# Kernel tuning notes

Measured on AMD Instinct MI355X. Metric: run time of the kernel, lower is better.

## Reference

```python
import jax, jax.numpy as jnp
import numpy as np
import math

B, T, D, H = 16, 512, 1024, 16
DK = D // H
MAX_LEN = 512          # RelativePositionBias default
LOCAL_WINDOW = 128


def setup_inputs() -> dict:
    key = jax.random.key(0)
    ks = jax.random.split(key, 6)
    x = jax.random.normal(ks[0], (B, T, D), dtype=jnp.float32)
    Wqkv = jax.random.normal(ks[1], (D, 3 * D), dtype=jnp.float32) * 0.02
    bqkv = jnp.zeros((3 * D,), dtype=jnp.float32)
    Wo = jax.random.normal(ks[2], (D, D), dtype=jnp.float32) * 0.02
    bo = jnp.zeros((D,), dtype=jnp.float32)
    rel_table = jax.random.normal(ks[3], (2 * MAX_LEN - 1, H), dtype=jnp.float32) * 0.02
    return {"x": x, "Wqkv": Wqkv, "bqkv": bqkv, "Wo": Wo, "bo": bo, "rel_table": rel_table}


def reference(x, Wqkv, bqkv, Wo, bo, rel_table):
    # QKV projection: [B,T,3D]
    qkv = x @ Wqkv + bqkv
    q, k, v = jnp.split(qkv, 3, axis=-1)
    # [B,T,D] -> [B,H,T,DK]
    def to_heads(t):
        return t.reshape(B, T, H, DK).transpose(0, 2, 1, 3)
    q, k, v = to_heads(q), to_heads(k), to_heads(v)

    # scaled dot-product scores: [B,H,T,T]
    scores = jnp.einsum('bhqd,bhkd->bhqk', q, k) / math.sqrt(DK)

    # relative position bias: dist[i,j] = j - i, clipped index in [0, 2*max_len-2]
    r = jnp.arange(T)
    idx = (r[None, :] - r[:, None]) + (MAX_LEN - 1)   # [T,T]
    bias = rel_table[idx]                              # [T,T,H]
    scores = scores + bias.transpose(2, 0, 1)[None]    # [1,H,T,T]

    # local window mask: keep j in [i-w, i+w]
    keep = jnp.abs(r[:, None] - r[None, :]) <= LOCAL_WINDOW  # [T,T]
    scores = jnp.where(keep[None, None], scores, -jnp.inf)

    attn = jax.nn.softmax(scores, axis=-1)
    ctx = jnp.einsum('bhqk,bhkd->bhqd', attn, v)       # [B,H,T,DK]
    ctx = ctx.transpose(0, 2, 1, 3).reshape(B, T, D)
    out = ctx @ Wo + bo
    return (out, attn)
```

## Files before the change

### kernel.cpp

```cpp
#include <hip/hip_runtime.h>
#include <math.h>

typedef unsigned short ushort_t;
typedef __bf16 bf16x8 __attribute__((ext_vector_type(8)));
typedef float f32x4 __attribute__((ext_vector_type(4)));
typedef ushort_t u16x8 __attribute__((ext_vector_type(8)));

#define BB 16
#define TT 512
#define DD 1024
#define HH 16
#define DKK 64
#define WIN 128
#define MAXLEN 512

#define TILE_M 64
#define JSPAN 320
#define NCHUNK 5

#define BK 32
#define TBUF (128 * BK)
#define BUFU (4 * TBUF)
#define KSTEPS (DD / BK)

#define ALS 72

#define GLOAD16(g, l)                                                                              \
    __builtin_amdgcn_global_load_lds((const __attribute__((address_space(1))) unsigned int*)(g),   \
                                     (__attribute__((address_space(3))) unsigned int*)(l), 16, 0, 0)

__device__ __forceinline__ ushort_t f2bf(float f) {
    union { float f; unsigned u; } x; x.f = f;
    unsigned r = x.u + 0x7fffu + ((x.u >> 16) & 1u);
    return (ushort_t)(r >> 16);
}
__device__ __forceinline__ float bf2f(ushort_t h) {
    union { unsigned u; float f; } x; x.u = ((unsigned)h) << 16;
    return x.f;
}

__device__ __forceinline__ int swi(int row, int col) {
    return row * ALS + (col ^ (((row >> 3) & 7) << 3));
}

__global__ __launch_bounds__(256) void conv_split(const float* __restrict__ src,
                                                  ushort_t* __restrict__ hi,
                                                  ushort_t* __restrict__ lo, int n4)
{
    const int i = blockIdx.x * 256 + threadIdx.x;
    if (i >= n4) return;
    float4 vf = ((const float4*)src)[i];
    ushort_t h0 = f2bf(vf.x), h1 = f2bf(vf.y), h2 = f2bf(vf.z), h3 = f2bf(vf.w);
    ushort4 hv = make_ushort4(h0, h1, h2, h3);
    ushort4 lv = make_ushort4(f2bf(vf.x - bf2f(h0)), f2bf(vf.y - bf2f(h1)),
                              f2bf(vf.z - bf2f(h2)), f2bf(vf.w - bf2f(h3)));
    ((ushort4*)hi)[i] = hv;
    ((ushort4*)lo)[i] = lv;
}

__global__ __launch_bounds__(256) void conv_split_T(const float* __restrict__ W,
                                                    ushort_t* __restrict__ hiT,
                                                    ushort_t* __restrict__ loT,
                                                    int K, int N)
{
    __shared__ ushort_t th[32][33], tl[32][33];
    const int n0 = blockIdx.x * 32, k0 = blockIdx.y * 32;
    const int tid = threadIdx.x;
    const int r = tid >> 3, c4 = (tid & 7) * 4;
    float4 vf = *(const float4*)&W[(size_t)(k0 + r) * N + n0 + c4];
    float vv[4] = {vf.x, vf.y, vf.z, vf.w};
#pragma unroll
    for (int j = 0; j < 4; ++j) {
        ushort_t h = f2bf(vv[j]);
        th[r][c4 + j] = h;
        tl[r][c4 + j] = f2bf(vv[j] - bf2f(h));
    }
    __syncthreads();
    ushort4 oh = make_ushort4(th[c4 + 0][r], th[c4 + 1][r], th[c4 + 2][r], th[c4 + 3][r]);
    ushort4 ol = make_ushort4(tl[c4 + 0][r], tl[c4 + 1][r], tl[c4 + 2][r], tl[c4 + 3][r]);
    *(ushort4*)&hiT[(size_t)(n0 + r) * K + k0 + c4] = oh;
    *(ushort4*)&loT[(size_t)(n0 + r) * K + k0 + c4] = ol;
}

__device__ __forceinline__ void mfma_mainloop(const ushort_t* __restrict__ Ah,
                                              const ushort_t* __restrict__ Al,
                                              const ushort_t* __restrict__ Bh,
                                              const ushort_t* __restrict__ Bl,
                                              int m0, int n0,
                                              ushort_t* smem, f32x4 (&acc)[4][4])
{
    const int tid = threadIdx.x;
    const int lane = tid & 63;
    const int w = tid >> 6;
    const int wm = (w >> 1) * 64, wn = (w & 1) * 64;
    const int c16 = lane & 15;
    const int quad = lane >> 4;

    const int lrow = lane >> 2, lq = lane & 3;
    const int r0 = w * 32, r1 = w * 32 + 16;
    const int row0 = r0 + lrow, row1 = r1 + lrow;
    const int qd0 = lq ^ ((row0 >> 1) & 3);
    const int qd1 = lq ^ ((row1 >> 1) & 3);
    const size_t a0 = (size_t)(m0 + row0) * DD + qd0 * 8;
    const size_t a1 = (size_t)(m0 + row1) * DD + qd1 * 8;
    const size_t b0 = (size_t)(n0 + row0) * DD + qd0 * 8;
    const size_t b1 = (size_t)(n0 + row1) * DD + qd1 * 8;

    auto STAGE = [&](int buf, int k0) {
        ushort_t* s_ = smem + buf * BUFU;
        GLOAD16(Ah + a0 + k0, (char*)s_ + r0 * 64);
        GLOAD16(Ah + a1 + k0, (char*)s_ + r1 * 64);
        GLOAD16(Al + a0 + k0, (char*)(s_ + TBUF) + r0 * 64);
        GLOAD16(Al + a1 + k0, (char*)(s_ + TBUF) + r1 * 64);
        GLOAD16(Bh + b0 + k0, (char*)(s_ + 2 * TBUF) + r0 * 64);
        GLOAD16(Bh + b1 + k0, (char*)(s_ + 2 * TBUF) + r1 * 64);
        GLOAD16(Bl + b0 + k0, (char*)(s_ + 3 * TBUF) + r0 * 64);
        GLOAD16(Bl + b1 + k0, (char*)(s_ + 3 * TBUF) + r1 * 64);
    };

    int aoff[4], boff[4];
#pragma unroll
    for (int mt = 0; mt < 4; ++mt) {
        const int row = wm + mt * 16 + c16;
        aoff[mt] = row * BK + ((quad ^ ((row >> 1) & 3)) * 8);
    }
#pragma unroll
    for (int nt = 0; nt < 4; ++nt) {
        const int row = wn + nt * 16 + c16;
        boff[nt] = row * BK + ((quad ^ ((row >> 1) & 3)) * 8);
    }

    STAGE(0, 0);
    for (int t = 0; t < KSTEPS; ++t) {
        const int cur = t & 1;
        if (t + 1 < KSTEPS) {
            STAGE(cur ^ 1, (t + 1) * BK);
            asm volatile("s_waitcnt vmcnt(8)" ::: "memory");
        } else {
            asm volatile("s_waitcnt vmcnt(0)" ::: "memory");
        }
        __builtin_amdgcn_sched_barrier(0);
        __builtin_amdgcn_s_barrier();

        const ushort_t* sAh = smem + cur * BUFU;
        const ushort_t* sAl = sAh + TBUF;
        const ushort_t* sBh = sAh + 2 * TBUF;
        const ushort_t* sBl = sAh + 3 * TBUF;
        bf16x8 ah[4], al[4];
#pragma unroll
        for (int mt = 0; mt < 4; ++mt) {
            ah[mt] = *(const bf16x8*)&sAh[aoff[mt]];
            al[mt] = *(const bf16x8*)&sAl[aoff[mt]];
        }
#pragma unroll
        for (int nt = 0; nt < 4; ++nt) {
            bf16x8 bh = *(const bf16x8*)&sBh[boff[nt]];
            bf16x8 bl = *(const bf16x8*)&sBl[boff[nt]];
#pragma unroll
            for (int mt = 0; mt < 4; ++mt) {
                acc[mt][nt] = __builtin_amdgcn_mfma_f32_16x16x32_bf16(ah[mt], bh, acc[mt][nt], 0, 0, 0);
                acc[mt][nt] = __builtin_amdgcn_mfma_f32_16x16x32_bf16(al[mt], bh, acc[mt][nt], 0, 0, 0);
                acc[mt][nt] = __builtin_amdgcn_mfma_f32_16x16x32_bf16(ah[mt], bl, acc[mt][nt], 0, 0, 0);
            }
        }
        __builtin_amdgcn_sched_barrier(0);
        __builtin_amdgcn_s_barrier();
    }
}

__global__ __launch_bounds__(256) void qkv_mfma(const ushort_t* __restrict__ xh,
                                                const ushort_t* __restrict__ xl,
                                                const ushort_t* __restrict__ wh,
                                                const ushort_t* __restrict__ wl,
                                                const float* __restrict__ bias,
                                                ushort_t* __restrict__ qh,
                                                ushort_t* __restrict__ ql,
                                                ushort_t* __restrict__ kh,
                                                ushort_t* __restrict__ kl,
                                                ushort_t* __restrict__ vh,
                                                ushort_t* __restrict__ vl)
{
    __shared__ ushort_t smem[2 * BUFU];
    f32x4 acc[4][4] = {};
    const int bid = blockIdx.x;
    const int swz = (bid & 7) * 192 + (bid >> 3);
    const int n0 = (swz % 24) * 128;
    const int m0 = (swz / 24) * 128;
    mfma_mainloop(xh, xl, wh, wl, m0, n0, smem, acc);

    const int tid = threadIdx.x, lane = tid & 63, w = tid >> 6;
    const int wm = (w >> 1) * 64, wn = (w & 1) * 64;
    const int c16 = lane & 15, rq = (lane >> 4) * 4;
#pragma unroll
    for (int mt = 0; mt < 4; ++mt)
#pragma unroll
        for (int nt = 0; nt < 4; ++nt)
#pragma unroll
            for (int r = 0; r < 4; ++r) {
                const int m = m0 + wm + mt * 16 + rq + r;
                const int n = n0 + wn + nt * 16 + c16;
                const float val = acc[mt][nt][r] + bias[n];
                const int bidx = m >> 9, t = m & (TT - 1);
                const int sel = n >> 10, d = n & (DD - 1);
                const int hd = d >> 6, dk = d & (DKK - 1);
                ushort_t* dsth = (sel == 0) ? qh : (sel == 1) ? kh : vh;
                ushort_t* dstl = (sel == 0) ? ql : (sel == 1) ? kl : vl;
                const size_t base = ((((size_t)bidx * HH + hd) * TT + t) * DKK) + dk;
                const ushort_t hi = f2bf(val);
                dsth[base] = hi;
                dstl[base] = f2bf(val - bf2f(hi));
            }
}

__global__ __launch_bounds__(256) void out_mfma(const ushort_t* __restrict__ ah,
                                                const ushort_t* __restrict__ al,
                                                const ushort_t* __restrict__ wh,
                                                const ushort_t* __restrict__ wl,
                                                const float* __restrict__ bias,
                                                float* __restrict__ out)
{
    __shared__ ushort_t smem[2 * BUFU];
    f32x4 acc[4][4] = {};
    const int bid = blockIdx.x;
    const int swz = (bid & 7) * 64 + (bid >> 3);
    const int n0 = (swz & 7) * 128;
    const int m0 = (swz >> 3) * 128;
    mfma_mainloop(ah, al, wh, wl, m0, n0, smem, acc);

    const int tid = threadIdx.x, lane = tid & 63, w = tid >> 6;
    const int wm = (w >> 1) * 64, wn = (w & 1) * 64;
    const int c16 = lane & 15, rq = (lane >> 4) * 4;
#pragma unroll
    for (int mt = 0; mt < 4; ++mt)
#pragma unroll
        for (int nt = 0; nt < 4; ++nt)
#pragma unroll
            for (int r = 0; r < 4; ++r) {
                const int m = m0 + wm + mt * 16 + rq + r;
                const int n = n0 + wn + nt * 16 + c16;
                out[(size_t)m * DD + n] = acc[mt][nt][r] + bias[n];
            }
}

__global__ __launch_bounds__(256) void attn_fused(const ushort_t* __restrict__ qh_g,
                                                  const ushort_t* __restrict__ ql_g,
                                                  const ushort_t* __restrict__ kh_g,
                                                  const ushort_t* __restrict__ kl_g,
                                                  const ushort_t* __restrict__ vh_g,
                                                  const ushort_t* __restrict__ vl_g,
                                                  const float* __restrict__ rel,
                                                  float* __restrict__ attn_out,
                                                  ushort_t* __restrict__ cxh,
                                                  ushort_t* __restrict__ cxl)
{
    const int gid = blockIdx.x;
    const int x = gid & 7;
    const int v = (gid >> 3) & 15;
    const int u = gid >> 7;
    const int it = v >> 1, mh = v & 1;
    const int bh_idx = u * 8 + x;
    const int h = bh_idx & 15, b = bh_idx >> 4;
    const int i0 = it * TILE_M;
    int jbase = i0 - WIN; if (jbase < 0) jbase = 0; if (jbase > TT - JSPAN) jbase = TT - JSPAN;
    const int irow0 = i0 + mh * 32;

    const int tid = threadIdx.x;
    const int lane = tid & 63, w = tid >> 6;
    const int c16 = lane & 15, quad = lane >> 4, rq = quad * 4;
    const int wnq = w * 16;

    __shared__ ushort_t sA0[32 * ALS], sA1[32 * ALS];
    __shared__ ushort_t sB0[64 * ALS], sB1[64 * ALS];
    __shared__ float bias_s[260];
    __shared__ float stats0[128], stats1[128];

    const size_t bh = (size_t)b * HH + h;
    const ushort_t* qhp = qh_g + (bh * TT + irow0) * DKK;
    const ushort_t* qlp = ql_g + (bh * TT + irow0) * DKK;
    const ushort_t* khp = kh_g + bh * TT * DKK;
    const ushort_t* klp = kl_g + bh * TT * DKK;
    const ushort_t* vhp = vh_g + bh * TT * DKK;
    const ushort_t* vlp = vl_g + bh * TT * DKK;
    float* arow = attn_out + (bh * TT + irow0) * TT;

    const int srow = tid >> 3, spart = (tid & 7) * 8;

    u16x8 kpre[2][2];
#pragma unroll
    for (int ii = 0; ii < 2; ++ii) {
        const size_t g = (size_t)(jbase + ii * 32 + srow) * DKK + spart;
        kpre[ii][0] = *(const u16x8*)&khp[g];
        kpre[ii][1] = *(const u16x8*)&klp[g];
    }

    {
        const float4 z = make_float4(0.f, 0.f, 0.f, 0.f);
        for (int idx = tid; idx < 32 * 48; idx += 256) {
            const int r  = idx / 48;
            const int c4 = idx - r * 48;
            const int col = (c4 * 4 < jbase) ? c4 * 4 : c4 * 4 + JSPAN;
            *(float4*)&arow[(size_t)r * TT + col] = z;
        }
    }
    if (tid < 257) bias_s[tid] = rel[(size_t)(tid + MAXLEN - 1 - 128) * HH + h];

    *(u16x8*)&sA0[swi(srow, spart)] = *(const u16x8*)&qhp[(size_t)srow * DKK + spart];
    *(u16x8*)&sA1[swi(srow, spart)] = *(const u16x8*)&qlp[(size_t)srow * DKK + spart];

    float s[NCHUNK][8];
#pragma unroll
    for (int c = 0; c < NCHUNK; ++c) {
#pragma unroll
        for (int ii = 0; ii < 2; ++ii) {
            *(u16x8*)&sB0[swi(ii * 32 + srow, spart)] = kpre[ii][0];
            *(u16x8*)&sB1[swi(ii * 32 + srow, spart)] = kpre[ii][1];
        }
        if (c + 1 < NCHUNK) {
#pragma unroll
            for (int ii = 0; ii < 2; ++ii) {
                const size_t g = (size_t)(jbase + (c + 1) * 64 + ii * 32 + srow) * DKK + spart;
                kpre[ii][0] = *(const u16x8*)&khp[g];
                kpre[ii][1] = *(const u16x8*)&klp[g];
            }
        }
        __syncthreads();
        f32x4 sacc[2] = {};
#pragma unroll
        for (int kk = 0; kk < 2; ++kk) {
            const int ku = kk * 32 + quad * 8;
            const bf16x8 kbh = *(const bf16x8*)&sB0[swi(wnq + c16, ku)];
            const bf16x8 kbl = *(const bf16x8*)&sB1[swi(wnq + c16, ku)];
#pragma unroll
            for (int mt = 0; mt < 2; ++mt) {
                const bf16x8 qah = *(const bf16x8*)&sA0[swi(mt * 16 + c16, ku)];
                const bf16x8 qal = *(const bf16x8*)&sA1[swi(mt * 16 + c16, ku)];
                sacc[mt] = __builtin_amdgcn_mfma_f32_16x16x32_bf16(qah, kbh, sacc[mt], 0, 0, 0);
                sacc[mt] = __builtin_amdgcn_mfma_f32_16x16x32_bf16(qal, kbh, sacc[mt], 0, 0, 0);
                sacc[mt] = __builtin_amdgcn_mfma_f32_16x16x32_bf16(qah, kbl, sacc[mt], 0, 0, 0);
            }
        }
        __syncthreads();
#pragma unroll
        for (int mt = 0; mt < 2; ++mt)
#pragma unroll
            for (int r = 0; r < 4; ++r) {
                const int i = irow0 + mt * 16 + rq + r;
                const int j = jbase + c * 64 + wnq + c16;
                const int d = j - i;
                const int bi = (d < -128) ? -128 : (d > 128 ? 128 : d);
                const float val = sacc[mt][r] * 0.125f + bias_s[bi + 128];
                s[c][mt * 4 + r] = (d >= -WIN && d <= WIN) ? val : -INFINITY;
            }
    }

    float mrow[2][4];
#pragma unroll
    for (int mt = 0; mt < 2; ++mt)
#pragma unroll
        for (int r = 0; r < 4; ++r) {
            float m = s[0][mt * 4 + r];
#pragma unroll
            for (int c = 1; c < NCHUNK; ++c) m = fmaxf(m, s[c][mt * 4 + r]);
            mrow[mt][r] = m;
        }
#pragma unroll
    for (int off = 1; off < 16; off <<= 1)
#pragma unroll
        for (int mt = 0; mt < 2; ++mt)
#pragma unroll
            for (int r = 0; r < 4; ++r)
                mrow[mt][r] = fmaxf(mrow[mt][r], __shfl_xor(mrow[mt][r], off));
    if (c16 == 0) {
#pragma unroll
        for (int mt = 0; mt < 2; ++mt)
#pragma unroll
            for (int r = 0; r < 4; ++r)
                stats0[(mt * 16 + rq + r) * 4 + w] = mrow[mt][r];
    }
    __syncthreads();
#pragma unroll
    for (int mt = 0; mt < 2; ++mt)
#pragma unroll
        for (int r = 0; r < 4; ++r) {
            const f32x4 q4 = *(const f32x4*)&stats0[(mt * 16 + rq + r) * 4];
            mrow[mt][r] = fmaxf(fmaxf(q4[0], q4[1]), fmaxf(q4[2], q4[3]));
        }
    float srow_[2][4];
#pragma unroll
    for (int mt = 0; mt < 2; ++mt)
#pragma unroll
        for (int r = 0; r < 4; ++r) srow_[mt][r] = 0.f;
#pragma unroll
    for (int c = 0; c < NCHUNK; ++c)
#pragma unroll
        for (int mt = 0; mt < 2; ++mt)
#pragma unroll
            for (int r = 0; r < 4; ++r) {
                const float e = __expf(s[c][mt * 4 + r] - mrow[mt][r]);
                s[c][mt * 4 + r] = e;
                srow_[mt][r] += e;
            }
#pragma unroll
    for (int off = 1; off < 16; off <<= 1)
#pragma unroll
        for (int mt = 0; mt < 2; ++mt)
#pragma unroll
            for (int r = 0; r < 4; ++r)
                srow_[mt][r] += __shfl_xor(srow_[mt][r], off);
    if (c16 == 0) {
#pragma unroll
        for (int mt = 0; mt < 2; ++mt)
#pragma unroll
            for (int r = 0; r < 4; ++r)
                stats1[(mt * 16 + rq + r) * 4 + w] = srow_[mt][r];
    }
    __syncthreads();
    float inv[2][4];
#pragma unroll
    for (int mt = 0; mt < 2; ++mt)
#pragma unroll
        for (int r = 0; r < 4; ++r) {
            const f32x4 q4 = *(const f32x4*)&stats1[(mt * 16 + rq + r) * 4];
            inv[mt][r] = 1.0f / (q4[0] + q4[1] + q4[2] + q4[3]);
        }

    u16x8 vpre[2][2];
#pragma unroll
    for (int ii = 0; ii < 2; ++ii) {
        const size_t g = (size_t)(jbase + ii * 32 + srow) * DKK + spart;
        vpre[ii][0] = *(const u16x8*)&vhp[g];
        vpre[ii][1] = *(const u16x8*)&vlp[g];
    }

    f32x4 oacc[2] = {};
#pragma unroll
    for (int c = 0; c < NCHUNK; ++c) {
        if (c > 0) __syncthreads();
#pragma unroll
        for (int mt = 0; mt < 2; ++mt)
#pragma unroll
            for (int r = 0; r < 4; ++r) {
                const int i = mt * 16 + rq + r;
                const float p = s[c][mt * 4 + r] * inv[mt][r];
                arow[(size_t)i * TT + jbase + c * 64 + wnq + c16] = p;
                const ushort_t ph = f2bf(p);
                const int col = (wnq + c16) ^ (((i >> 3) & 7) << 3);
                sA0[i * ALS + col] = ph;
                sA1[i * ALS + col] = f2bf(p - bf2f(ph));
            }
#pragma unroll
        for (int ii = 0; ii < 2; ++ii) {
            const int jr = ii * 32 + srow;
#pragma unroll
            for (int e = 0; e < 8; ++e) {
                const int dk = spart + e;
                const int idx = dk * ALS + (jr ^ (((dk >> 3) & 7) << 3));
                sB0[idx] = vpre[ii][0][e];
                sB1[idx] = vpre[ii][1][e];
            }
        }
        if (c + 1 < NCHUNK) {
#pragma unroll
            for (int ii = 0; ii < 2; ++ii) {
                const size_t g = (size_t)(jbase + (c + 1) * 64 + ii * 32 + srow) * DKK + spart;
                vpre[ii][0] = *(const u16x8*)&vhp[g];
                vpre[ii][1] = *(const u16x8*)&vlp[g];
            }
        }
        __syncthreads();
#pragma unroll
        for (int kk = 0; kk < 2; ++kk) {
            const int ku = kk * 32 + quad * 8;
            const bf16x8 vbh = *(const bf16x8*)&sB0[swi(wnq + c16, ku)];
            const bf16x8 vbl = *(const bf16x8*)&sB1[swi(wnq + c16, ku)];
#pragma unroll
            for (int mt = 0; mt < 2; ++mt) {
                const bf16x8 pah = *(const bf16x8*)&sA0[swi(mt * 16 + c16, ku)];
                const bf16x8 pal = *(const bf16x8*)&sA1[swi(mt * 16 + c16, ku)];
                oacc[mt] = __builtin_amdgcn_mfma_f32_16x16x32_bf16(pah, vbh, oacc[mt], 0, 0, 0);
                oacc[mt] = __builtin_amdgcn_mfma_f32_16x16x32_bf16(pal, vbh, oacc[mt], 0, 0, 0);
                oacc[mt] = __builtin_amdgcn_mfma_f32_16x16x32_bf16(pah, vbl, oacc[mt], 0, 0, 0);
            }
        }
    }

#pragma unroll
    for (int mt = 0; mt < 2; ++mt)
#pragma unroll
        for (int r = 0; r < 4; ++r) {
            const float val = oacc[mt][r];
            const int i = mt * 16 + rq + r;
            const int dk = wnq + c16;
            const ushort_t hh2 = f2bf(val);
            const size_t off = (((size_t)b * TT + irow0 + i) * HH + h) * DKK + dk;
            cxh[off] = hh2;
            cxl[off] = f2bf(val - bf2f(hh2));
        }
}

extern "C" void kernel_launch(void* const* d_in, const int* in_sizes, int n_in,
                              void* d_out, int out_size, void* d_ws, size_t ws_size,
                              hipStream_t stream)
{
    const float* x    = (const float*)d_in[0];
    const float* Wqkv = (const float*)d_in[1];
    const float* bqkv = (const float*)d_in[2];
    const float* Wo   = (const float*)d_in[3];
    const float* bo   = (const float*)d_in[4];
    const float* rel  = (const float*)d_in[5];

    float* out  = (float*)d_out;
    float* attn = out + (size_t)BB * TT * DD;

    const size_t per = (size_t)BB * HH * TT * DKK;
    ushort_t* qh = (ushort_t*)d_ws;
    ushort_t* ql = qh + per;
    ushort_t* kh = ql + per;
    ushort_t* kl = kh + per;
    ushort_t* vh = kl + per;
    ushort_t* vl = vh + per;
    ushort_t* xh = vl + per;
    ushort_t* xl = xh + per;
    ushort_t* Wqh = xl + per;
    ushort_t* Wql = Wqh + (size_t)DD * 3 * DD;
    ushort_t* cxh = xh;
    ushort_t* cxl = xl;
    ushort_t* Woh = vh;
    ushort_t* Wol = Woh + (size_t)DD * DD;

    const int n4x = BB * TT * DD / 4;

    conv_split<<<dim3((n4x + 255) / 256), 256, 0, stream>>>(x, xh, xl, n4x);
    conv_split_T<<<dim3(3 * DD / 32, DD / 32), 256, 0, stream>>>(Wqkv, Wqh, Wql, DD, 3 * DD);
    qkv_mfma<<<dim3(1536), 256, 0, stream>>>(xh, xl, Wqh, Wql, bqkv, qh, ql, kh, kl, vh, vl);
    attn_fused<<<dim3(4096), 256, 0, stream>>>(qh, ql, kh, kl, vh, vl, rel, attn, cxh, cxl);
    conv_split_T<<<dim3(DD / 32, DD / 32), 256, 0, stream>>>(Wo, Woh, Wol, DD, DD);
    out_mfma<<<dim3(512), 256, 0, stream>>>(cxh, cxl, Woh, Wol, bo, out);
}
```

Baseline: 625.7 us.

## Switch split-bf16 emulation to fp16 two-term splits, dropping low parts

All MFMA paths move from bf16 hi/lo triple products to fp16 with a two-product scheme (A hi+lo times B hi only). Weights, K, V and the P matrix in the PV product are kept as single fp16 values, which removes their lo buffers, their loads and LDS traffic, and one third of the MFMAs in every GEMM and in attention. The intent is to lean on fp16's extra mantissa bits so the result stays within fp32-reference tolerance. The cost is reduced precision: fp16's narrow range risks overflow or underflow, and error grows from the dropped low terms.

```diff
diff --git a/kernel.cpp b/kernel.cpp
--- a/kernel.cpp
+++ b/kernel.cpp
@@ -1,10 +1,10 @@
 #include <hip/hip_runtime.h>
 #include <math.h>
 
-typedef unsigned short ushort_t;
-typedef __bf16 bf16x8 __attribute__((ext_vector_type(8)));
+typedef _Float16 half_t;
+typedef _Float16 f16x8 __attribute__((ext_vector_type(8)));
+typedef _Float16 f16x4 __attribute__((ext_vector_type(4)));
 typedef float f32x4 __attribute__((ext_vector_type(4)));
-typedef ushort_t u16x8 __attribute__((ext_vector_type(8)));
 
 #define BB 16
 #define TT 512
@@ -20,7 +20,7 @@
 
 #define BK 32
 #define TBUF (128 * BK)
-#define BUFU (4 * TBUF)
+#define BUFU (3 * TBUF)
 #define KSTEPS (DD / BK)
 
 #define ALS 72
@@ -29,65 +29,54 @@
     __builtin_amdgcn_global_load_lds((const __attribute__((address_space(1))) unsigned int*)(g),   \
                                      (__attribute__((address_space(3))) unsigned int*)(l), 16, 0, 0)
 
-__device__ __forceinline__ ushort_t f2bf(float f) {
-    union { float f; unsigned u; } x; x.f = f;
-    unsigned r = x.u + 0x7fffu + ((x.u >> 16) & 1u);
-    return (ushort_t)(r >> 16);
-}
-__device__ __forceinline__ float bf2f(ushort_t h) {
-    union { unsigned u; float f; } x; x.u = ((unsigned)h) << 16;
-    return x.f;
-}
+__device__ __forceinline__ half_t f2h(float f) { return (half_t)f; }
+__device__ __forceinline__ float  h2f(half_t h) { return (float)h; }
 
 __device__ __forceinline__ int swi(int row, int col) {
     return row * ALS + (col ^ (((row >> 3) & 7) << 3));
 }
 
 __global__ __launch_bounds__(256) void conv_split(const float* __restrict__ src,
-                                                  ushort_t* __restrict__ hi,
-                                                  ushort_t* __restrict__ lo, int n4)
+                                                  half_t* __restrict__ hi,
+                                                  half_t* __restrict__ lo, int n4)
 {
     const int i = blockIdx.x * 256 + threadIdx.x;
     if (i >= n4) return;
     float4 vf = ((const float4*)src)[i];
-    ushort_t h0 = f2bf(vf.x), h1 = f2bf(vf.y), h2 = f2bf(vf.z), h3 = f2bf(vf.w);
-    ushort4 hv = make_ushort4(h0, h1, h2, h3);
-    ushort4 lv = make_ushort4(f2bf(vf.x - bf2f(h0)), f2bf(vf.y - bf2f(h1)),
-                              f2bf(vf.z - bf2f(h2)), f2bf(vf.w - bf2f(h3)));
-    ((ushort4*)hi)[i] = hv;
-    ((ushort4*)lo)[i] = lv;
-}
-
-__global__ __launch_bounds__(256) void conv_split_T(const float* __restrict__ W,
-                                                    ushort_t* __restrict__ hiT,
-                                                    ushort_t* __restrict__ loT,
-                                                    int K, int N)
-{
-    __shared__ ushort_t th[32][33], tl[32][33];
+    float vv[4] = {vf.x, vf.y, vf.z, vf.w};
+    f16x4 hv, lv;
+#pragma unroll
+    for (int j = 0; j < 4; ++j) {
+        const half_t h = f2h(vv[j]);
+        hv[j] = h;
+        lv[j] = f2h(vv[j] - h2f(h));
+    }
+    *(f16x4*)&hi[(size_t)i * 4] = hv;
+    *(f16x4*)&lo[(size_t)i * 4] = lv;
+}
+
+__global__ __launch_bounds__(256) void conv_T(const float* __restrict__ W,
+                                              half_t* __restrict__ hiT,
+                                              int K, int N)
+{
+    __shared__ half_t th[32][33];
     const int n0 = blockIdx.x * 32, k0 = blockIdx.y * 32;
     const int tid = threadIdx.x;
     const int r = tid >> 3, c4 = (tid & 7) * 4;
     float4 vf = *(const float4*)&W[(size_t)(k0 + r) * N + n0 + c4];
     float vv[4] = {vf.x, vf.y, vf.z, vf.w};
 #pragma unroll
-    for (int j = 0; j < 4; ++j) {
-        ushort_t h = f2bf(vv[j]);
-        th[r][c4 + j] = h;
-        tl[r][c4 + j] = f2bf(vv[j] - bf2f(h));
-    }
+    for (int j = 0; j < 4; ++j) th[r][c4 + j] = f2h(vv[j]);
     __syncthreads();
-    ushort4 oh = make_ushort4(th[c4 + 0][r], th[c4 + 1][r], th[c4 + 2][r], th[c4 + 3][r]);
-    ushort4 ol = make_ushort4(tl[c4 + 0][r], tl[c4 + 1][r], tl[c4 + 2][r], tl[c4 + 3][r]);
-    *(ushort4*)&hiT[(size_t)(n0 + r) * K + k0 + c4] = oh;
-    *(ushort4*)&loT[(size_t)(n0 + r) * K + k0 + c4] = ol;
-}
-
-__device__ __forceinline__ void mfma_mainloop(const ushort_t* __restrict__ Ah,
-                                              const ushort_t* __restrict__ Al,
-                                              const ushort_t* __restrict__ Bh,
-                                              const ushort_t* __restrict__ Bl,
+    f16x4 oh = {th[c4 + 0][r], th[c4 + 1][r], th[c4 + 2][r], th[c4 + 3][r]};
+    *(f16x4*)&hiT[(size_t)(n0 + r) * K + k0 + c4] = oh;
+}
+
+__device__ __forceinline__ void mfma_mainloop(const half_t* __restrict__ Ah,
+                                              const half_t* __restrict__ Al,
+                                              const half_t* __restrict__ Bh,
                                               int m0, int n0,
-                                              ushort_t* smem, f32x4 (&acc)[4][4])
+                                              half_t* smem, f32x4 (&acc)[4][4])
 {
     const int tid = threadIdx.x;
     const int lane = tid & 63;
@@ -107,15 +96,13 @@
     const size_t b1 = (size_t)(n0 + row1) * DD + qd1 * 8;
 
     auto STAGE = [&](int buf, int k0) {
-        ushort_t* s_ = smem + buf * BUFU;
+        half_t* s_ = smem + buf * BUFU;
         GLOAD16(Ah + a0 + k0, (char*)s_ + r0 * 64);
         GLOAD16(Ah + a1 + k0, (char*)s_ + r1 * 64);
         GLOAD16(Al + a0 + k0, (char*)(s_ + TBUF) + r0 * 64);
         GLOAD16(Al + a1 + k0, (char*)(s_ + TBUF) + r1 * 64);
         GLOAD16(Bh + b0 + k0, (char*)(s_ + 2 * TBUF) + r0 * 64);
         GLOAD16(Bh + b1 + k0, (char*)(s_ + 2 * TBUF) + r1 * 64);
-        GLOAD16(Bl + b0 + k0, (char*)(s_ + 3 * TBUF) + r0 * 64);
-        GLOAD16(Bl + b1 + k0, (char*)(s_ + 3 * TBUF) + r1 * 64);
     };
 
     int aoff[4], boff[4];
@@ -135,32 +122,29 @@
         const int cur = t & 1;
         if (t + 1 < KSTEPS) {
             STAGE(cur ^ 1, (t + 1) * BK);
-            asm volatile("s_waitcnt vmcnt(8)" ::: "memory");
+            asm volatile("s_waitcnt vmcnt(6)" ::: "memory");
         } else {
             asm volatile("s_waitcnt vmcnt(0)" ::: "memory");
         }
         __builtin_amdgcn_sched_barrier(0);
         __builtin_amdgcn_s_barrier();
 
-        const ushort_t* sAh = smem + cur * BUFU;
-        const ushort_t* sAl = sAh + TBUF;
-        const ushort_t* sBh = sAh + 2 * TBUF;
-        const ushort_t* sBl = sAh + 3 * TBUF;
-        bf16x8 ah[4], al[4];
+        const half_t* sAh = smem + cur * BUFU;
+        const half_t* sAl = sAh + TBUF;
+        const half_t* sBh = sAh + 2 * TBUF;
+        f16x8 ah[4], al[4];
 #pragma unroll
         for (int mt = 0; mt < 4; ++mt) {
-            ah[mt] = *(const bf16x8*)&sAh[aoff[mt]];
-            al[mt] = *(const bf16x8*)&sAl[aoff[mt]];
+            ah[mt] = *(const f16x8*)&sAh[aoff[mt]];
+            al[mt] = *(const f16x8*)&sAl[aoff[mt]];
         }
 #pragma unroll
         for (int nt = 0; nt < 4; ++nt) {
-            bf16x8 bh = *(const bf16x8*)&sBh[boff[nt]];
-            bf16x8 bl = *(const bf16x8*)&sBl[boff[nt]];
+            f16x8 bh = *(const f16x8*)&sBh[boff[nt]];
 #pragma unroll
             for (int mt = 0; mt < 4; ++mt) {
-                acc[mt][nt] = __builtin_amdgcn_mfma_f32_16x16x32_bf16(ah[mt], bh, acc[mt][nt], 0, 0, 0);
-                acc[mt][nt] = __builtin_amdgcn_mfma_f32_16x16x32_bf16(al[mt], bh, acc[mt][nt], 0, 0, 0);
-                acc[mt][nt] = __builtin_amdgcn_mfma_f32_16x16x32_bf16(ah[mt], bl, acc[mt][nt], 0, 0, 0);
+                acc[mt][nt] = __builtin_amdgcn_mfma_f32_16x16x32_f16(ah[mt], bh, acc[mt][nt], 0, 0, 0);
+                acc[mt][nt] = __builtin_amdgcn_mfma_f32_16x16x32_f16(al[mt], bh, acc[mt][nt], 0, 0, 0);
             }
         }
         __builtin_amdgcn_sched_barrier(0);
@@ -168,25 +152,22 @@
     }
 }
 
-__global__ __launch_bounds__(256) void qkv_mfma(const ushort_t* __restrict__ xh,
-                                                const ushort_t* __restrict__ xl,
-                                                const ushort_t* __restrict__ wh,
-                                                const ushort_t* __restrict__ wl,
+__global__ __launch_bounds__(256) void qkv_mfma(const half_t* __restrict__ xh,
+                                                const half_t* __restrict__ xl,
+                                                const half_t* __restrict__ wh,
                                                 const float* __restrict__ bias,
-                                                ushort_t* __restrict__ qh,
-                                                ushort_t* __restrict__ ql,
-                                                ushort_t* __restrict__ kh,
-                                                ushort_t* __restrict__ kl,
-                                                ushort_t* __restrict__ vh,
-                                                ushort_t* __restrict__ vl)
-{
-    __shared__ ushort_t smem[2 * BUFU];
+                                                half_t* __restrict__ qh,
+                                                half_t* __restrict__ ql,
+                                                half_t* __restrict__ kh,
+                                                half_t* __restrict__ vh)
+{
+    __shared__ half_t smem[2 * BUFU];
     f32x4 acc[4][4] = {};
     const int bid = blockIdx.x;
     const int swz = (bid & 7) * 192 + (bid >> 3);
     const int n0 = (swz % 24) * 128;
     const int m0 = (swz / 24) * 128;
-    mfma_mainloop(xh, xl, wh, wl, m0, n0, smem, acc);
+    mfma_mainloop(xh, xl, wh, m0, n0, smem, acc);
 
     const int tid = threadIdx.x, lane = tid & 63, w = tid >> 6;
     const int wm = (w >> 1) * 64, wn = (w & 1) * 64;
@@ -203,29 +184,32 @@
                 const int bidx = m >> 9, t = m & (TT - 1);
                 const int sel = n >> 10, d = n & (DD - 1);
                 const int hd = d >> 6, dk = d & (DKK - 1);
-                ushort_t* dsth = (sel == 0) ? qh : (sel == 1) ? kh : vh;
-                ushort_t* dstl = (sel == 0) ? ql : (sel == 1) ? kl : vl;
                 const size_t base = ((((size_t)bidx * HH + hd) * TT + t) * DKK) + dk;
-                const ushort_t hi = f2bf(val);
-                dsth[base] = hi;
-                dstl[base] = f2bf(val - bf2f(hi));
-            }
-}
-
-__global__ __launch_bounds__(256) void out_mfma(const ushort_t* __restrict__ ah,
-                                                const ushort_t* __restrict__ al,
-                                                const ushort_t* __restrict__ wh,
-                                                const ushort_t* __restrict__ wl,
+                const half_t hv = f2h(val);
+                if (sel == 0) {
+                    qh[base] = hv;
+                    ql[base] = f2h(val - h2f(hv));
+                } else if (sel == 1) {
+                    kh[base] = hv;
+                } else {
+                    vh[base] = hv;
+                }
+            }
+}
+
+__global__ __launch_bounds__(256) void out_mfma(const half_t* __restrict__ ah,
+                                                const half_t* __restrict__ al,
+                                                const half_t* __restrict__ wh,
                                                 const float* __restrict__ bias,
                                                 float* __restrict__ out)
 {
-    __shared__ ushort_t smem[2 * BUFU];
+    __shared__ half_t smem[2 * BUFU];
     f32x4 acc[4][4] = {};
     const int bid = blockIdx.x;
     const int swz = (bid & 7) * 64 + (bid >> 3);
     const int n0 = (swz & 7) * 128;
     const int m0 = (swz >> 3) * 128;
-    mfma_mainloop(ah, al, wh, wl, m0, n0, smem, acc);
+    mfma_mainloop(ah, al, wh, m0, n0, smem, acc);
 
     const int tid = threadIdx.x, lane = tid & 63, w = tid >> 6;
     const int wm = (w >> 1) * 64, wn = (w & 1) * 64;
@@ -242,16 +226,14 @@
             }
 }
 
-__global__ __launch_bounds__(256) void attn_fused(const ushort_t* __restrict__ qh_g,
-                                                  const ushort_t* __restrict__ ql_g,
-                                                  const ushort_t* __restrict__ kh_g,
-                                                  const ushort_t* __restrict__ kl_g,
-                                                  const ushort_t* __restrict__ vh_g,
-                                                  const ushort_t* __restrict__ vl_g,
+__global__ __launch_bounds__(256) void attn_fused(const half_t* __restrict__ qh_g,
+                                                  const half_t* __restrict__ ql_g,
+                                                  const half_t* __restrict__ kh_g,
+                                                  const half_t* __restrict__ vh_g,
                                                   const float* __restrict__ rel,
                                                   float* __restrict__ attn_out,
-                                                  ushort_t* __restrict__ cxh,
-                                                  ushort_t* __restrict__ cxl)
+                                                  half_t* __restrict__ cxh,
+                                                  half_t* __restrict__ cxl)
 {
     const int gid = blockIdx.x;
     const int x = gid & 7;
@@ -269,29 +251,24 @@
     const int c16 = lane & 15, quad = lane >> 4, rq = quad * 4;
     const int wnq = w * 16;
 
-    __shared__ ushort_t sA0[32 * ALS], sA1[32 * ALS];
-    __shared__ ushort_t sB0[64 * ALS], sB1[64 * ALS];
+    __shared__ half_t sA0[32 * ALS], sA1[32 * ALS];
+    __shared__ half_t sB0[64 * ALS];
     __shared__ float bias_s[260];
     __shared__ float stats0[128], stats1[128];
 
     const size_t bh = (size_t)b * HH + h;
-    const ushort_t* qhp = qh_g + (bh * TT + irow0) * DKK;
-    const ushort_t* qlp = ql_g + (bh * TT + irow0) * DKK;
-    const ushort_t* khp = kh_g + bh * TT * DKK;
-    const ushort_t* klp = kl_g + bh * TT * DKK;
-    const ushort_t* vhp = vh_g + bh * TT * DKK;
-    const ushort_t* vlp = vl_g + bh * TT * DKK;
+    const half_t* qhp = qh_g + (bh * TT + irow0) * DKK;
+    const half_t* qlp = ql_g + (bh * TT + irow0) * DKK;
+    const half_t* khp = kh_g + bh * TT * DKK;
+    const half_t* vhp = vh_g + bh * TT * DKK;
     float* arow = attn_out + (bh * TT + irow0) * TT;
 
     const int srow = tid >> 3, spart = (tid & 7) * 8;
 
-    u16x8 kpre[2][2];
-#pragma unroll
-    for (int ii = 0; ii < 2; ++ii) {
-        const size_t g = (size_t)(jbase + ii * 32 + srow) * DKK + spart;
-        kpre[ii][0] = *(const u16x8*)&khp[g];
-        kpre[ii][1] = *(const u16x8*)&klp[g];
-    }
+    f16x8 kpre[2];
+#pragma unroll
+    for (int ii = 0; ii < 2; ++ii)
+        kpre[ii] = *(const f16x8*)&khp[(size_t)(jbase + ii * 32 + srow) * DKK + spart];
 
     {
         const float4 z = make_float4(0.f, 0.f, 0.f, 0.f);
@@ -304,39 +281,32 @@
     }
     if (tid < 257) bias_s[tid] = rel[(size_t)(tid + MAXLEN - 1 - 128) * HH + h];
 
-    *(u16x8*)&sA0[swi(srow, spart)] = *(const u16x8*)&qhp[(size_t)srow * DKK + spart];
-    *(u16x8*)&sA1[swi(srow, spart)] = *(const u16x8*)&qlp[(size_t)srow * DKK + spart];
+    *(f16x8*)&sA0[swi(srow, spart)] = *(const f16x8*)&qhp[(size_t)srow * DKK + spart];
+    *(f16x8*)&sA1[swi(srow, spart)] = *(const f16x8*)&qlp[(size_t)srow * DKK + spart];
 
     float s[NCHUNK][8];
 #pragma unroll
     for (int c = 0; c < NCHUNK; ++c) {
 #pragma unroll
-        for (int ii = 0; ii < 2; ++ii) {
-            *(u16x8*)&sB0[swi(ii * 32 + srow, spart)] = kpre[ii][0];
-            *(u16x8*)&sB1[swi(ii * 32 + srow, spart)] = kpre[ii][1];
-        }
+        for (int ii = 0; ii < 2; ++ii)
+            *(f16x8*)&sB0[swi(ii * 32 + srow, spart)] = kpre[ii];
         if (c + 1 < NCHUNK) {
 #pragma unroll
-            for (int ii = 0; ii < 2; ++ii) {
-                const size_t g = (size_t)(jbase + (c + 1) * 64 + ii * 32 + srow) * DKK + spart;
-                kpre[ii][0] = *(const u16x8*)&khp[g];
-                kpre[ii][1] = *(const u16x8*)&klp[g];
-            }
+            for (int ii = 0; ii < 2; ++ii)
+                kpre[ii] = *(const f16x8*)&khp[(size_t)(jbase + (c + 1) * 64 + ii * 32 + srow) * DKK + spart];
         }
         __syncthreads();
         f32x4 sacc[2] = {};
 #pragma unroll
         for (int kk = 0; kk < 2; ++kk) {
             const int ku = kk * 32 + quad * 8;
-            const bf16x8 kbh = *(const bf16x8*)&sB0[swi(wnq + c16, ku)];
-            const bf16x8 kbl = *(const bf16x8*)&sB1[swi(wnq + c16, ku)];
+            const f16x8 kb = *(const f16x8*)&sB0[swi(wnq + c16, ku)];
 #pragma unroll
             for (int mt = 0; mt < 2; ++mt) {
-                const bf16x8 qah = *(const bf16x8*)&sA0[swi(mt * 16 + c16, ku)];
-                const bf16x8 qal = *(const bf16x8*)&sA1[swi(mt * 16 + c16, ku)];
-                sacc[mt] = __builtin_amdgcn_mfma_f32_16x16x32_bf16(qah, kbh, sacc[mt], 0, 0, 0);
-                sacc[mt] = __builtin_amdgcn_mfma_f32_16x16x32_bf16(qal, kbh, sacc[mt], 0, 0, 0);
-                sacc[mt] = __builtin_amdgcn_mfma_f32_16x16x32_bf16(qah, kbl, sacc[mt], 0, 0, 0);
+                const f16x8 qah = *(const f16x8*)&sA0[swi(mt * 16 + c16, ku)];
+                const f16x8 qal = *(const f16x8*)&sA1[swi(mt * 16 + c16, ku)];
+                sacc[mt] = __builtin_amdgcn_mfma_f32_16x16x32_f16(qah, kb, sacc[mt], 0, 0, 0);
+                sacc[mt] = __builtin_amdgcn_mfma_f32_16x16x32_f16(qal, kb, sacc[mt], 0, 0, 0);
             }
         }
         __syncthreads();
@@ -424,13 +394,10 @@
             inv[mt][r] = 1.0f / (q4[0] + q4[1] + q4[2] + q4[3]);
         }
 
-    u16x8 vpre[2][2];
-#pragma unroll
-    for (int ii = 0; ii < 2; ++ii) {
-        const size_t g = (size_t)(jbase + ii * 32 + srow) * DKK + spart;
-        vpre[ii][0] = *(const u16x8*)&vhp[g];
-        vpre[ii][1] = *(const u16x8*)&vlp[g];
-    }
+    f16x8 vpre[2];
+#pragma unroll
+    for (int ii = 0; ii < 2; ++ii)
+        vpre[ii] = *(const f16x8*)&vhp[(size_t)(jbase + ii * 32 + srow) * DKK + spart];
 
     f32x4 oacc[2] = {};
 #pragma unroll
@@ -443,10 +410,8 @@
                 const int i = mt * 16 + rq + r;
                 const float p = s[c][mt * 4 + r] * inv[mt][r];
                 arow[(size_t)i * TT + jbase + c * 64 + wnq + c16] = p;
-                const ushort_t ph = f2bf(p);
                 const int col = (wnq + c16) ^ (((i >> 3) & 7) << 3);
-                sA0[i * ALS + col] = ph;
-                sA1[i * ALS + col] = f2bf(p - bf2f(ph));
+                sA0[i * ALS + col] = f2h(p);
             }
 #pragma unroll
         for (int ii = 0; ii < 2; ++ii) {
@@ -454,32 +419,23 @@
 #pragma unroll
             for (int e = 0; e < 8; ++e) {
                 const int dk = spart + e;
-                const int idx = dk * ALS + (jr ^ (((dk >> 3) & 7) << 3));
-                sB0[idx] = vpre[ii][0][e];
-                sB1[idx] = vpre[ii][1][e];
+                sB0[dk * ALS + (jr ^ (((dk >> 3) & 7) << 3))] = vpre[ii][e];
             }
         }
         if (c + 1 < NCHUNK) {
 #pragma unroll
-            for (int ii = 0; ii < 2; ++ii) {
-                const size_t g = (size_t)(jbase + (c + 1) * 64 + ii * 32 + srow) * DKK + spart;
-                vpre[ii][0] = *(const u16x8*)&vhp[g];
-                vpre[ii][1] = *(const u16x8*)&vlp[g];
-            }
+            for (int ii = 0; ii < 2; ++ii)
+                vpre[ii] = *(const f16x8*)&vhp[(size_t)(jbase + (c + 1) * 64 + ii * 32 + srow) * DKK + spart];
         }
         __syncthreads();
 #pragma unroll
         for (int kk = 0; kk < 2; ++kk) {
             const int ku = kk * 32 + quad * 8;
-            const bf16x8 vbh = *(const bf16x8*)&sB0[swi(wnq + c16, ku)];
-            const bf16x8 vbl = *(const bf16x8*)&sB1[swi(wnq + c16, ku)];
+            const f16x8 vb = *(const f16x8*)&sB0[swi(wnq + c16, ku)];
 #pragma unroll
             for (int mt = 0; mt < 2; ++mt) {
-                const bf16x8 pah = *(const bf16x8*)&sA0[swi(mt * 16 + c16, ku)];
-                const bf16x8 pal = *(const bf16x8*)&sA1[swi(mt * 16 + c16, ku)];
-                oacc[mt] = __builtin_amdgcn_mfma_f32_16x16x32_bf16(pah, vbh, oacc[mt], 0, 0, 0);
-                oacc[mt] = __builtin_amdgcn_mfma_f32_16x16x32_bf16(pal, vbh, oacc[mt], 0, 0, 0);
-                oacc[mt] = __builtin_amdgcn_mfma_f32_16x16x32_bf16(pah, vbl, oacc[mt], 0, 0, 0);
+                const f16x8 pa = *(const f16x8*)&sA0[swi(mt * 16 + c16, ku)];
+                oacc[mt] = __builtin_amdgcn_mfma_f32_16x16x32_f16(pa, vb, oacc[mt], 0, 0, 0);
             }
         }
     }
@@ -491,10 +447,10 @@
             const float val = oacc[mt][r];
             const int i = mt * 16 + rq + r;
             const int dk = wnq + c16;
-            const ushort_t hh2 = f2bf(val);
+            const half_t hv = f2h(val);
             const size_t off = (((size_t)b * TT + irow0 + i) * HH + h) * DKK + dk;
-            cxh[off] = hh2;
-            cxl[off] = f2bf(val - bf2f(hh2));
+            cxh[off] = hv;
+            cxl[off] = f2h(val - h2f(hv));
         }
 }
 
@@ -513,27 +469,23 @@
     float* attn = out + (size_t)BB * TT * DD;
 
     const size_t per = (size_t)BB * HH * TT * DKK;
-    ushort_t* qh = (ushort_t*)d_ws;
-    ushort_t* ql = qh + per;
-    ushort_t* kh = ql + per;
-    ushort_t* kl = kh + per;
-    ushort_t* vh = kl + per;
-    ushort_t* vl = vh + per;
-    ushort_t* xh = vl + per;
-    ushort_t* xl = xh + per;
-    ushort_t* Wqh = xl + per;
-    ushort_t* Wql = Wqh + (size_t)DD * 3 * DD;
-    ushort_t* cxh = xh;
-    ushort_t* cxl = xl;
-    ushort_t* Woh = vh;
-    ushort_t* Wol = Woh + (size_t)DD * DD;
+    half_t* qh = (half_t*)d_ws;
+    half_t* ql = qh + per;
+    half_t* kh = ql + per;
+    half_t* vh = kh + per;
+    half_t* xh = vh + per;
+    half_t* xl = xh + per;
+    half_t* Wqh = xl + per;
+    half_t* cxh = xh;
+    half_t* cxl = xl;
+    half_t* Woh = kh;
 
     const int n4x = BB * TT * DD / 4;
 
     conv_split<<<dim3((n4x + 255) / 256), 256, 0, stream>>>(x, xh, xl, n4x);
-    conv_split_T<<<dim3(3 * DD / 32, DD / 32), 256, 0, stream>>>(Wqkv, Wqh, Wql, DD, 3 * DD);
-    qkv_mfma<<<dim3(1536), 256, 0, stream>>>(xh, xl, Wqh, Wql, bqkv, qh, ql, kh, kl, vh, vl);
-    attn_fused<<<dim3(4096), 256, 0, stream>>>(qh, ql, kh, kl, vh, vl, rel, attn, cxh, cxl);
-    conv_split_T<<<dim3(DD / 32, DD / 32), 256, 0, stream>>>(Wo, Woh, Wol, DD, DD);
-    out_mfma<<<dim3(512), 256, 0, stream>>>(cxh, cxl, Woh, Wol, bo, out);
-}
+    conv_T<<<dim3(3 * DD / 32, DD / 32), 256, 0, stream>>>(Wqkv, Wqh, DD, 3 * DD);
+    qkv_mfma<<<dim3(1536), 256, 0, stream>>>(xh, xl, Wqh, bqkv, qh, ql, kh, vh);
+    attn_fused<<<dim3(4096), 256, 0, stream>>>(qh, ql, kh, vh, rel, attn, cxh, cxl);
+    conv_T<<<dim3(DD / 32, DD / 32), 256, 0, stream>>>(Wo, Woh, DD, DD);
+    out_mfma<<<dim3(512), 256, 0, stream>>>(cxh, cxl, Woh, bo, out);
+}
```

Result: faster. 544.5 us (-13.0%).
